# Kernel tuning notes

Measured on AMD Instinct MI355X. Metric: run time of the kernel, lower is better.

Reference implementation:

```python
import jax, jax.numpy as jnp
from jax import lax
import numpy as np

B = 512
IN_CAPS, OUT_CAPS, IN_DIM, OUT_DIM, ITERS = 32 * 6 * 6, 10, 8, 16, 3
EPS = 1e-8


def setup_inputs() -> dict:
    key = jax.random.key(0)
    ks = jax.random.split(key, 12)
    inp = {
        "x": jax.random.normal(ks[0], (B, 1, 28, 28), dtype=jnp.float32),
        "conv1_w": jax.random.normal(ks[1], (256, 1, 9, 9), dtype=jnp.float32) * 0.05,
        "conv1_b": jnp.zeros((256,), dtype=jnp.float32),
        "conv2_w": jax.random.normal(ks[2], (256, 256, 9, 9), dtype=jnp.float32) * 0.02,
        "conv2_b": jnp.zeros((256,), dtype=jnp.float32),
        "W": jax.random.normal(ks[3], (IN_CAPS, OUT_CAPS, IN_DIM, OUT_DIM), dtype=jnp.float32) * 0.1,
        "d1_w": jax.random.normal(ks[4], (OUT_DIM * OUT_CAPS, 512), dtype=jnp.float32) * 0.05,
        "d1_b": jnp.zeros((512,), dtype=jnp.float32),
        "d2_w": jax.random.normal(ks[5], (512, 1024), dtype=jnp.float32) * 0.05,
        "d2_b": jnp.zeros((1024,), dtype=jnp.float32),
        "d3_w": jax.random.normal(ks[6], (1024, 28 * 28), dtype=jnp.float32) * 0.05,
        "d3_b": jnp.zeros((28 * 28,), dtype=jnp.float32),
    }
    return inp


def _squash(s):
    # s2/(1+s2) * s/sqrt(s2+eps), norm over last dim
    s2 = jnp.sum(s * s, axis=-1, keepdims=True)
    return s2 / (1.0 + s2) * (s / jnp.sqrt(s2 + EPS))


def _conv(x, w, b, stride):
    y = lax.conv_general_dilated(x, w, (stride, stride), "VALID",
                                 dimension_numbers=("NCHW", "OIHW", "NCHW"))
    return y + b[None, :, None, None]


def reference(x, conv1_w, conv1_b, conv2_w, conv2_b, W,
              d1_w, d1_b, d2_w, d2_b, d3_w, d3_b):
    h = jax.nn.relu(_conv(x, conv1_w, conv1_b, 1))          # [B,256,20,20]
    h = _conv(h, conv2_w, conv2_b, 2)                       # [B,256,6,6]
    u = h.reshape(h.shape[0], 8, IN_CAPS).transpose(0, 2, 1)  # [B,1152,8]
    u = _squash(u)

    # dynamic routing
    u_hat = jnp.einsum("ijnm,bin->bijm", W, u)              # [B,1152,10,16]
    b_log = jnp.zeros((u.shape[0], IN_CAPS, OUT_CAPS), dtype=u.dtype)
    v = None
    for _ in range(ITERS):
        c = jax.nn.softmax(b_log, axis=1)                   # over in_capsules (as original)
        s = jnp.einsum("bij,bijm->bjm", c, u_hat)           # [B,10,16]
        v = _squash(s)
        b_log = b_log + jnp.einsum("bjm,bijm->bij", v, u_hat)
    caps = v                                                # [B,10,16]

    pred = jnp.argmax(jnp.sum(caps * caps, axis=-1), axis=-1)  # [B]
    mask = jax.lax.stop_gradient(jax.nn.one_hot(pred, OUT_CAPS, dtype=caps.dtype))
    dec_in = (caps * mask[:, :, None]).reshape(caps.shape[0], -1)  # [B,160]
    r = jax.nn.relu(dec_in @ d1_w + d1_b)
    r = jax.nn.relu(r @ d2_w + d2_b)
    r = jax.nn.sigmoid(r @ d3_w + d3_b)
    recon = r.reshape(-1, 1, 28, 28)
    return caps, recon, pred
```

## Files before the change

### kernel.cpp

```cpp
#include <hip/hip_runtime.h>

#define CAPS_EPS 1e-8f

typedef __attribute__((ext_vector_type(8))) short short8;
typedef __attribute__((ext_vector_type(4))) float f32x4;

__device__ inline ushort bf16_rn(float f) {
    uint u = __float_as_uint(f);
    u += 0x7fff + ((u >> 16) & 1);
    return (ushort)(u >> 16);
}
__device__ inline float bf16_f(ushort h) { return __uint_as_float((uint)h << 16); }

__device__ __forceinline__ void gld16(const void* g, void* l) {
    __builtin_amdgcn_global_load_lds(
        (const __attribute__((address_space(1))) unsigned int*)g,
        (__attribute__((address_space(3))) unsigned int*)l, 16, 0, 0);
}


__global__ __launch_bounds__(256) void k_wt2(const float* __restrict__ w2,
                                             ushort* __restrict__ wBhi,
                                             ushort* __restrict__ wBlo) {
    int n = blockIdx.x;
    int c = threadIdx.x;
    const float* src = w2 + (size_t)n * 20736 + c * 81;
    ushort* dh = wBhi + (size_t)n * 20736 + c;
    ushort* dl = wBlo + (size_t)n * 20736 + c;
    for (int t = 0; t < 81; ++t) {
        float f = src[t];
        ushort hi = bf16_rn(f);
        ushort lo = bf16_rn(f - bf16_f(hi));
        dh[t * 256] = hi;
        dl[t * 256] = lo;
    }
}

__global__ __launch_bounds__(256) void k_conv1(const float* __restrict__ x,
                                               const float* __restrict__ w1,
                                               const float* __restrict__ b1,
                                               ushort* __restrict__ h1hi,
                                               ushort* __restrict__ h1lo) {
    int blk = blockIdx.x;
    int b = blk / 5, strip = blk % 5;
    int y0 = strip * 4;
    int c = threadIdx.x;
    float w[81];
#pragma unroll
    for (int k = 0; k < 81; ++k) w[k] = w1[c * 81 + k];
    float bias = b1[c];
    const float* xb = x + (size_t)b * 784;
    for (int dy = 0; dy < 4; ++dy) {
        int y = y0 + dy;
        float acc[20];
#pragma unroll
        for (int i = 0; i < 20; ++i) acc[i] = bias;
#pragma unroll
        for (int ky = 0; ky < 9; ++ky) {
            float xr[28];
            const float4* xp = reinterpret_cast<const float4*>(xb + (y + ky) * 28);
#pragma unroll
            for (int q = 0; q < 7; ++q) {
                float4 v = xp[q];
                xr[q * 4 + 0] = v.x; xr[q * 4 + 1] = v.y;
                xr[q * 4 + 2] = v.z; xr[q * 4 + 3] = v.w;
            }
#pragma unroll
            for (int kx = 0; kx < 9; ++kx) {
                float wv = w[ky * 9 + kx];
#pragma unroll
                for (int xo = 0; xo < 20; ++xo)
                    acc[xo] = fmaf(xr[xo + kx], wv, acc[xo]);
            }
        }
#pragma unroll
        for (int xo = 0; xo < 20; ++xo) {
            float a = fmaxf(acc[xo], 0.f);
            ushort hi = bf16_rn(a);
            ushort lo = bf16_rn(a - bf16_f(hi));
            size_t o = ((size_t)(b * 20 + y) * 20 + xo) * 256 + c;
            h1hi[o] = hi;
            h1lo[o] = lo;
        }
    }
}

__global__ __launch_bounds__(256) void k_h2init(const float* __restrict__ b2,
                                                float* __restrict__ h2) {
    h2[(size_t)blockIdx.x * 256 + threadIdx.x] = b2[threadIdx.x];
}

__global__ __launch_bounds__(256) void k_zero4(float* __restrict__ p) {
    reinterpret_cast<float4*>(p)[(size_t)blockIdx.x * 256 + threadIdx.x] = make_float4(0, 0, 0, 0);
}

__global__ __launch_bounds__(256, 4) void k_conv2m(const ushort* __restrict__ h1hi,
                                                   const ushort* __restrict__ h1lo,
                                                   const ushort* __restrict__ wBhi,
                                                   const ushort* __restrict__ wBlo,
                                                   float* __restrict__ h2) {
    __shared__ ushort Ahi[128 * 32];
    __shared__ ushort Alo[128 * 32];
    __shared__ ushort Bhi[128 * 32];
    __shared__ ushort Blo[128 * 32];
    int tid = threadIdx.x;
    int m0 = blockIdx.x * 128;
    int n0 = blockIdx.y * 128;
    int kbase = blockIdx.z * 2592;

    int wv = tid >> 6, lane = tid & 63;

    int r0 = wv * 32 + (lane >> 2);
    int r1 = r0 + 16;
    int cq = (lane & 3) * 8;
    int mA0 = m0 + r0, mA1 = m0 + r1;
    int mb0 = mA0 / 36, mp0 = mA0 - mb0 * 36;
    int mb1 = mA1 / 36, mp1 = mA1 - mb1 * 36;
    size_t a0 = ((size_t)mb0 * 400 + (mp0 / 6) * 40 + (mp0 % 6) * 2) * 256 + cq;
    size_t a1 = ((size_t)mb1 * 400 + (mp1 / 6) * 40 + (mp1 % 6) * 2) * 256 + cq;
    size_t b0 = (size_t)(n0 + r0) * 20736 + cq;
    size_t b1 = (size_t)(n0 + r1) * 20736 + cq;
    int ldsw = wv * 1024;

    int mhalf = (wv >> 1) * 64, nhalf = (wv & 1) * 64;
    int lrow = lane & 15, quad = lane >> 4;

    f32x4 acc[4][4];
#pragma unroll
    for (int a = 0; a < 4; ++a)
#pragma unroll
        for (int bq = 0; bq < 4; ++bq) acc[a][bq] = (f32x4){0.f, 0.f, 0.f, 0.f};

    for (int ks = 0; ks < 81; ++ks) {
        int k = kbase + ks * 32;
        int t = k >> 8, cc = k & 255;
        int ky = t / 9, kx = t - ky * 9;
        size_t koffA = (size_t)(ky * 5120 + kx * 256 + cc);

        __syncthreads();
        gld16(h1hi + a0 + koffA, &Ahi[ldsw]);
        gld16(h1hi + a1 + koffA, &Ahi[ldsw + 512]);
        gld16(h1lo + a0 + koffA, &Alo[ldsw]);
        gld16(h1lo + a1 + koffA, &Alo[ldsw + 512]);
        gld16(wBhi + b0 + k, &Bhi[ldsw]);
        gld16(wBhi + b1 + k, &Bhi[ldsw + 512]);
        gld16(wBlo + b0 + k, &Blo[ldsw]);
        gld16(wBlo + b1 + k, &Blo[ldsw + 512]);
        __syncthreads();

        short8 bh[4], blo[4];
#pragma unroll
        for (int tn = 0; tn < 4; ++tn) {
            int off = (nhalf + tn * 16 + lrow) * 32 + quad * 8;
            bh[tn] = *reinterpret_cast<short8*>(&Bhi[off]);
            blo[tn] = *reinterpret_cast<short8*>(&Blo[off]);
        }
#pragma unroll
        for (int tm = 0; tm < 4; ++tm) {
            int off = (mhalf + tm * 16 + lrow) * 32 + quad * 8;
            short8 ah = *reinterpret_cast<short8*>(&Ahi[off]);
            short8 al = *reinterpret_cast<short8*>(&Alo[off]);
#pragma unroll
            for (int tn = 0; tn < 4; ++tn) {
                acc[tm][tn] = __builtin_amdgcn_mfma_f32_16x16x32_bf16(ah, bh[tn], acc[tm][tn], 0, 0, 0);
                acc[tm][tn] = __builtin_amdgcn_mfma_f32_16x16x32_bf16(ah, blo[tn], acc[tm][tn], 0, 0, 0);
                acc[tm][tn] = __builtin_amdgcn_mfma_f32_16x16x32_bf16(al, bh[tn], acc[tm][tn], 0, 0, 0);
            }
        }
    }

#pragma unroll
    for (int tm = 0; tm < 4; ++tm) {
        int mrow = m0 + mhalf + tm * 16 + quad * 4;
#pragma unroll
        for (int tn = 0; tn < 4; ++tn) {
            int ncol = n0 + nhalf + tn * 16 + lrow;
#pragma unroll
            for (int r = 0; r < 4; ++r)
                atomicAdd(&h2[(size_t)(mrow + r) * 256 + ncol], acc[tm][tn][r]);
        }
    }
}

__global__ __launch_bounds__(256) void k_squashT(const float* __restrict__ h2,
                                                 float* __restrict__ uT) {
    int i = blockIdx.x;
    int b = blockIdx.y * 256 + threadIdx.x;
    int g = i / 36, s = i - g * 36;
    const float* hp = h2 + ((size_t)b * 36 + s) * 256 + g;
    float val[8];
    float s2 = 0.f;
#pragma unroll
    for (int n = 0; n < 8; ++n) {
        val[n] = hp[n * 32];
        s2 = fmaf(val[n], val[n], s2);
    }
    float scale = s2 / ((1.f + s2) * sqrtf(s2 + CAPS_EPS));
#pragma unroll
    for (int n = 0; n < 8; ++n)
        uT[((size_t)i * 8 + n) * 512 + b] = val[n] * scale;
}

__global__ __launch_bounds__(256) void k_s(const float* __restrict__ Wc,
                                           const float* __restrict__ uT,
                                           const float* __restrict__ bl,
                                           const float* __restrict__ Z,
                                           float* __restrict__ sT,
                                           int first) {
    __shared__ float lw[8 * 1280];
    int tid = threadIdx.x;
    int i0 = blockIdx.x * 8;
    int b = blockIdx.y * 128 + (tid & 127);
    int mh = tid >> 7;
    const float* wg = Wc + (size_t)i0 * 1280;
#pragma unroll
    for (int r = 0; r < 10; ++r) {
        int q4 = (r * 256 + tid) * 4;
        *reinterpret_cast<float4*>(&lw[q4]) = *reinterpret_cast<const float4*>(wg + q4);
    }
    __syncthreads();
    float rzs[10];
    if (!first) {
#pragma unroll
        for (int j = 0; j < 10; ++j) rzs[j] = 1.0f / Z[j * 512 + b];
    }
    float acc[80];
#pragma unroll
    for (int q = 0; q < 80; ++q) acc[q] = 0.f;
    for (int di = 0; di < 8; ++di) {
        int i = i0 + di;
        float ur[8];
#pragma unroll
        for (int n = 0; n < 8; ++n) ur[n] = uT[((size_t)i * 8 + n) * 512 + b];
#pragma unroll
        for (int j = 0; j < 10; ++j) {
            float c;
            if (first) c = (1.0f / 1152.0f);
            else c = expf(bl[((size_t)i * 10 + j) * 512 + b]) * rzs[j];
            const float* wp = &lw[((di * 10 + j) * 8) * 16 + mh * 8];
#pragma unroll
            for (int mm = 0; mm < 8; ++mm) {
                float uh = 0.f;
#pragma unroll
                for (int n = 0; n < 8; ++n) uh = fmaf(wp[n * 16 + mm], ur[n], uh);
                acc[j * 8 + mm] = fmaf(c, uh, acc[j * 8 + mm]);
            }
        }
    }
#pragma unroll
    for (int j = 0; j < 10; ++j)
#pragma unroll
        for (int mm = 0; mm < 8; ++mm)
            atomicAdd(&sT[(j * 16 + mh * 8 + mm) * 512 + b], acc[j * 8 + mm]);
}

__global__ __launch_bounds__(256) void k_v(const float* __restrict__ sT,
                                           float* __restrict__ v,
                                           float* __restrict__ vT,
                                           float* __restrict__ sTz,
                                           float* __restrict__ Z) {
    int idx = blockIdx.x * 256 + threadIdx.x;
    int j = idx >> 9;
    int b = idx & 511;
    float sv[16];
    float s2 = 0.f;
#pragma unroll
    for (int m = 0; m < 16; ++m) {
        sv[m] = sT[(j * 16 + m) * 512 + b];
        s2 = fmaf(sv[m], sv[m], s2);
    }
    float scale = s2 / ((1.f + s2) * sqrtf(s2 + CAPS_EPS));
#pragma unroll
    for (int m = 0; m < 16; ++m) {
        float val = sv[m] * scale;
        v[(size_t)b * 160 + j * 16 + m] = val;
        vT[(j * 16 + m) * 512 + b] = val;
        sTz[(j * 16 + m) * 512 + b] = 0.f;
    }
    Z[idx] = 0.f;
}

__global__ __launch_bounds__(256) void k_bupd(const float* __restrict__ Wc,
                                              const float* __restrict__ uT,
                                              const float* __restrict__ vT,
                                              float* __restrict__ bl,
                                              float* __restrict__ Z) {
    __shared__ float lw[8 * 1280];
    int tid = threadIdx.x;
    int i0 = blockIdx.x * 8;
    int b = blockIdx.y * 128 + (tid & 127);
    int ih = tid >> 7;
    const float* wg = Wc + (size_t)i0 * 1280;
#pragma unroll
    for (int r = 0; r < 10; ++r) {
        int q4 = (r * 256 + tid) * 4;
        *reinterpret_cast<float4*>(&lw[q4]) = *reinterpret_cast<const float4*>(wg + q4);
    }
    __syncthreads();
    float ur[4][8];
#pragma unroll
    for (int ii = 0; ii < 4; ++ii) {
        int i = i0 + ih * 4 + ii;
#pragma unroll
        for (int n = 0; n < 8; ++n) ur[ii][n] = uT[((size_t)i * 8 + n) * 512 + b];
    }
    for (int j = 0; j < 10; ++j) {
        float vj[16];
#pragma unroll
        for (int m = 0; m < 16; ++m) vj[m] = vT[(j * 16 + m) * 512 + b];
        float zp = 0.f;
#pragma unroll
        for (int ii = 0; ii < 4; ++ii) {
            int di = ih * 4 + ii;
            const float* wp = &lw[((di * 10 + j) * 8) * 16];
            float t = 0.f;
#pragma unroll
            for (int n = 0; n < 8; ++n) {
                float wvv = 0.f;
#pragma unroll
                for (int m = 0; m < 16; ++m) wvv = fmaf(wp[n * 16 + m], vj[m], wvv);
                t = fmaf(ur[ii][n], wvv, t);
            }
            size_t idx = ((size_t)(i0 + di) * 10 + j) * 512 + b;
            float nb = bl[idx] + t;
            bl[idx] = nb;
            zp += expf(nb);
        }
        atomicAdd(&Z[j * 512 + b], zp);
    }
}

__global__ __launch_bounds__(256) void k_pred(const float* __restrict__ v,
                                              float* __restrict__ out,
                                              float* __restrict__ dec,
                                              int pred_off) {
    int b = blockIdx.x, t = threadIdx.x;
    __shared__ float sq[160];
    __shared__ float nrm[10];
    __shared__ int ip;
    float val = 0.f;
    if (t < 160) {
        val = v[(size_t)b * 160 + t];
        out[(size_t)b * 160 + t] = val;
        sq[t] = val * val;
    }
    __syncthreads();
    if (t < 10) {
        float s = 0.f;
#pragma unroll
        for (int k = 0; k < 16; ++k) s += sq[t * 16 + k];
        nrm[t] = s;
    }
    __syncthreads();
    if (t == 0) {
        float best = nrm[0];
        int bi = 0;
        for (int j = 1; j < 10; ++j)
            if (nrm[j] > best) { best = nrm[j]; bi = j; }
        ip = bi;
        out[(size_t)pred_off + b] = (float)bi;
    }
    __syncthreads();
    if (t < 160) dec[(size_t)b * 160 + t] = ((t >> 4) == ip) ? val : 0.f;
}

template <int ACT>
__global__ __launch_bounds__(256) void k_gemm(const float* __restrict__ A,
                                              const float* __restrict__ B,
                                              const float* __restrict__ bias,
                                              float* __restrict__ C,
                                              int M, int K, int N) {
    __shared__ float As[16 * 64];
    __shared__ float Bs[16 * 64];
    int tid = threadIdx.x;
    int m0 = blockIdx.y * 64, n0 = blockIdx.x * 64;
    int arow = tid >> 2, akq = (tid & 3) * 4;
    int brow = tid >> 4, bcol = (tid & 15) * 4;
    int ty = tid >> 4, tx = tid & 15;
    float acc[4][4];
#pragma unroll
    for (int r = 0; r < 4; ++r)
#pragma unroll
        for (int q = 0; q < 4; ++q) acc[r][q] = 0.f;
    for (int k0 = 0; k0 < K; k0 += 16) {
        float4 av = *reinterpret_cast<const float4*>(A + (size_t)(m0 + arow) * K + k0 + akq);
        float4 bv = make_float4(0, 0, 0, 0);
        if (n0 + bcol < N)
            bv = *reinterpret_cast<const float4*>(B + (size_t)(k0 + brow) * N + n0 + bcol);
        __syncthreads();
        As[(akq + 0) * 64 + arow] = av.x;
        As[(akq + 1) * 64 + arow] = av.y;
        As[(akq + 2) * 64 + arow] = av.z;
        As[(akq + 3) * 64 + arow] = av.w;
        *reinterpret_cast<float4*>(&Bs[brow * 64 + bcol]) = bv;
        __syncthreads();
#pragma unroll
        for (int kk = 0; kk < 16; ++kk) {
            float4 a4 = *reinterpret_cast<float4*>(&As[kk * 64 + ty * 4]);
            float4 b4 = *reinterpret_cast<float4*>(&Bs[kk * 64 + tx * 4]);
            float ar[4] = {a4.x, a4.y, a4.z, a4.w};
            float br[4] = {b4.x, b4.y, b4.z, b4.w};
#pragma unroll
            for (int r = 0; r < 4; ++r)
#pragma unroll
                for (int q = 0; q < 4; ++q)
                    acc[r][q] = fmaf(ar[r], br[q], acc[r][q]);
        }
    }
#pragma unroll
    for (int r = 0; r < 4; ++r) {
        int mm = m0 + ty * 4 + r;
#pragma unroll
        for (int q = 0; q < 4; ++q) {
            int nn = n0 + tx * 4 + q;
            if (nn < N) {
                float val = acc[r][q] + bias[nn];
                if (ACT == 0) val = fmaxf(val, 0.f);
                else val = 1.f / (1.f + expf(-val));
                C[(size_t)mm * N + nn] = val;
            }
        }
    }
}

extern "C" void kernel_launch(void* const* d_in, const int* in_sizes, int n_in,
                              void* d_out, int out_size, void* d_ws, size_t ws_size,
                              hipStream_t stream) {
    const float* x   = (const float*)d_in[0];
    const float* w1  = (const float*)d_in[1];
    const float* b1  = (const float*)d_in[2];
    const float* w2  = (const float*)d_in[3];
    const float* b2  = (const float*)d_in[4];
    const float* Wc  = (const float*)d_in[5];
    const float* d1w = (const float*)d_in[6];
    const float* d1b = (const float*)d_in[7];
    const float* d2w = (const float*)d_in[8];
    const float* d2b = (const float*)d_in[9];
    const float* d3w = (const float*)d_in[10];
    const float* d3b = (const float*)d_in[11];
    float* out = (float*)d_out;

    ushort* wBhi = (ushort*)d_ws;
    ushort* wBlo = wBhi + 5308416;
    ushort* h1hi = (ushort*)((char*)d_ws + 21233664);
    ushort* h1lo = h1hi + 52428800;
    float*  h2   = (float*)((char*)d_ws + 230948864);

    float* post = (float*)((char*)d_ws + 21233664);
    float* uT  = post + 4718592;
    float* bl  = post + 9437184;
    float* sT  = post + 15335424;
    float* Z   = post + 15417344;
    float* v   = post + 15422464;
    float* vT  = post + 15504384;
    float* dec = post + 15586304;
    float* r1  = post + 15668224;
    float* r2  = post + 15930368;

    int pred_off = out_size - 512;

    k_wt2<<<256, 256, 0, stream>>>(w2, wBhi, wBlo);
    k_conv1<<<2560, 256, 0, stream>>>(x, w1, b1, h1hi, h1lo);
    k_h2init<<<18432, 256, 0, stream>>>(b2, h2);
    k_conv2m<<<dim3(144, 2, 8), 256, 0, stream>>>(h1hi, h1lo, wBhi, wBlo, h2);
    k_zero4<<<5845, 256, 0, stream>>>(bl);
    k_squashT<<<dim3(1152, 2), 256, 0, stream>>>(h2, uT);

    for (int it = 0; it < 3; ++it) {
        k_s<<<dim3(144, 4), 256, 0, stream>>>(Wc, uT, bl, Z, sT, it == 0 ? 1 : 0);
        k_v<<<20, 256, 0, stream>>>(sT, v, vT, sT, Z);
        if (it < 2) k_bupd<<<dim3(144, 4), 256, 0, stream>>>(Wc, uT, vT, bl, Z);
    }

    k_pred<<<512, 256, 0, stream>>>(v, out, dec, pred_off);
    k_gemm<0><<<dim3(8, 8), 256, 0, stream>>>(dec, d1w, d1b, r1, 512, 160, 512);
    k_gemm<0><<<dim3(16, 8), 256, 0, stream>>>(r1, d2w, d2b, r2, 512, 512, 1024);
    k_gemm<1><<<dim3(13, 8), 256, 0, stream>>>(r2, d3w, d3b, out + 81920, 512, 1024, 784);
}
```

Before: 1.649 ms.

## Widen conv2 GEMM tile to cover all 256 output channels per block

The conv2 implicit GEMM block tile grows from 128x128 to 128x256, so each block covers every output channel. Each A (activation) tile is then loaded from global memory once instead of twice, and the grid drops from 2304 to 1152 blocks. The cost is a doubled accumulator array (128 floats per thread), double the B LDS buffers, and launch bounds lowered to 2 blocks per CU. That means higher register pressure and lower occupancy, with only about 4.5 waves of blocks over the CUs.

```diff
diff --git a/kernel.cpp b/kernel.cpp
--- a/kernel.cpp
+++ b/kernel.cpp
@@ -94,42 +94,42 @@
     reinterpret_cast<float4*>(p)[(size_t)blockIdx.x * 256 + threadIdx.x] = make_float4(0, 0, 0, 0);
 }
 
-__global__ __launch_bounds__(256, 4) void k_conv2m(const ushort* __restrict__ h1hi,
+__global__ __launch_bounds__(256, 2) void k_conv2m(const ushort* __restrict__ h1hi,
                                                    const ushort* __restrict__ h1lo,
                                                    const ushort* __restrict__ wBhi,
                                                    const ushort* __restrict__ wBlo,
                                                    float* __restrict__ h2) {
     __shared__ ushort Ahi[128 * 32];
     __shared__ ushort Alo[128 * 32];
-    __shared__ ushort Bhi[128 * 32];
-    __shared__ ushort Blo[128 * 32];
+    __shared__ ushort Bhi[256 * 32];
+    __shared__ ushort Blo[256 * 32];
     int tid = threadIdx.x;
     int m0 = blockIdx.x * 128;
-    int n0 = blockIdx.y * 128;
-    int kbase = blockIdx.z * 2592;
+    int kbase = blockIdx.y * 2592;
 
     int wv = tid >> 6, lane = tid & 63;
-
-    int r0 = wv * 32 + (lane >> 2);
-    int r1 = r0 + 16;
     int cq = (lane & 3) * 8;
-    int mA0 = m0 + r0, mA1 = m0 + r1;
+
+    int ra = wv * 32 + (lane >> 2);
+    int mA0 = m0 + ra, mA1 = mA0 + 16;
     int mb0 = mA0 / 36, mp0 = mA0 - mb0 * 36;
     int mb1 = mA1 / 36, mp1 = mA1 - mb1 * 36;
     size_t a0 = ((size_t)mb0 * 400 + (mp0 / 6) * 40 + (mp0 % 6) * 2) * 256 + cq;
     size_t a1 = ((size_t)mb1 * 400 + (mp1 / 6) * 40 + (mp1 % 6) * 2) * 256 + cq;
-    size_t b0 = (size_t)(n0 + r0) * 20736 + cq;
-    size_t b1 = (size_t)(n0 + r1) * 20736 + cq;
-    int ldsw = wv * 1024;
-
-    int mhalf = (wv >> 1) * 64, nhalf = (wv & 1) * 64;
+    int ldsA = wv * 1024;
+
+    int rb = wv * 64 + (lane >> 2);
+    size_t bB = (size_t)rb * 20736 + cq;
+    int ldsB = wv * 2048;
+
+    int mhalf = (wv >> 1) * 64, nhalf = (wv & 1) * 128;
     int lrow = lane & 15, quad = lane >> 4;
 
-    f32x4 acc[4][4];
+    f32x4 acc[4][8];
 #pragma unroll
     for (int a = 0; a < 4; ++a)
 #pragma unroll
-        for (int bq = 0; bq < 4; ++bq) acc[a][bq] = (f32x4){0.f, 0.f, 0.f, 0.f};
+        for (int bq = 0; bq < 8; ++bq) acc[a][bq] = (f32x4){0.f, 0.f, 0.f, 0.f};
 
     for (int ks = 0; ks < 81; ++ks) {
         int k = kbase + ks * 32;
@@ -138,33 +138,35 @@
         size_t koffA = (size_t)(ky * 5120 + kx * 256 + cc);
 
         __syncthreads();
-        gld16(h1hi + a0 + koffA, &Ahi[ldsw]);
-        gld16(h1hi + a1 + koffA, &Ahi[ldsw + 512]);
-        gld16(h1lo + a0 + koffA, &Alo[ldsw]);
-        gld16(h1lo + a1 + koffA, &Alo[ldsw + 512]);
-        gld16(wBhi + b0 + k, &Bhi[ldsw]);
-        gld16(wBhi + b1 + k, &Bhi[ldsw + 512]);
-        gld16(wBlo + b0 + k, &Blo[ldsw]);
-        gld16(wBlo + b1 + k, &Blo[ldsw + 512]);
+        gld16(h1hi + a0 + koffA, &Ahi[ldsA]);
+        gld16(h1hi + a1 + koffA, &Ahi[ldsA + 512]);
+        gld16(h1lo + a0 + koffA, &Alo[ldsA]);
+        gld16(h1lo + a1 + koffA, &Alo[ldsA + 512]);
+#pragma unroll
+        for (int q = 0; q < 4; ++q) {
+            size_t bo = bB + (size_t)q * 331776 + k;
+            gld16(wBhi + bo, &Bhi[ldsB + q * 512]);
+            gld16(wBlo + bo, &Blo[ldsB + q * 512]);
+        }
         __syncthreads();
 
-        short8 bh[4], blo[4];
-#pragma unroll
-        for (int tn = 0; tn < 4; ++tn) {
-            int off = (nhalf + tn * 16 + lrow) * 32 + quad * 8;
-            bh[tn] = *reinterpret_cast<short8*>(&Bhi[off]);
-            blo[tn] = *reinterpret_cast<short8*>(&Blo[off]);
-        }
+        short8 ah[4], al[4];
 #pragma unroll
         for (int tm = 0; tm < 4; ++tm) {
             int off = (mhalf + tm * 16 + lrow) * 32 + quad * 8;
-            short8 ah = *reinterpret_cast<short8*>(&Ahi[off]);
-            short8 al = *reinterpret_cast<short8*>(&Alo[off]);
-#pragma unroll
-            for (int tn = 0; tn < 4; ++tn) {
-                acc[tm][tn] = __builtin_amdgcn_mfma_f32_16x16x32_bf16(ah, bh[tn], acc[tm][tn], 0, 0, 0);
-                acc[tm][tn] = __builtin_amdgcn_mfma_f32_16x16x32_bf16(ah, blo[tn], acc[tm][tn], 0, 0, 0);
-                acc[tm][tn] = __builtin_amdgcn_mfma_f32_16x16x32_bf16(al, bh[tn], acc[tm][tn], 0, 0, 0);
+            ah[tm] = *reinterpret_cast<short8*>(&Ahi[off]);
+            al[tm] = *reinterpret_cast<short8*>(&Alo[off]);
+        }
+#pragma unroll
+        for (int tn = 0; tn < 8; ++tn) {
+            int off = (nhalf + tn * 16 + lrow) * 32 + quad * 8;
+            short8 bh = *reinterpret_cast<short8*>(&Bhi[off]);
+            short8 bl2 = *reinterpret_cast<short8*>(&Blo[off]);
+#pragma unroll
+            for (int tm = 0; tm < 4; ++tm) {
+                acc[tm][tn] = __builtin_amdgcn_mfma_f32_16x16x32_bf16(ah[tm], bh, acc[tm][tn], 0, 0, 0);
+                acc[tm][tn] = __builtin_amdgcn_mfma_f32_16x16x32_bf16(ah[tm], bl2, acc[tm][tn], 0, 0, 0);
+                acc[tm][tn] = __builtin_amdgcn_mfma_f32_16x16x32_bf16(al[tm], bh, acc[tm][tn], 0, 0, 0);
             }
         }
     }
@@ -173,8 +175,8 @@
     for (int tm = 0; tm < 4; ++tm) {
         int mrow = m0 + mhalf + tm * 16 + quad * 4;
 #pragma unroll
-        for (int tn = 0; tn < 4; ++tn) {
-            int ncol = n0 + nhalf + tn * 16 + lrow;
+        for (int tn = 0; tn < 8; ++tn) {
+            int ncol = nhalf + tn * 16 + lrow;
 #pragma unroll
             for (int r = 0; r < 4; ++r)
                 atomicAdd(&h2[(size_t)(mrow + r) * 256 + ncol], acc[tm][tn][r]);
@@ -462,7 +464,7 @@
     k_wt2<<<256, 256, 0, stream>>>(w2, wBhi, wBlo);
     k_conv1<<<2560, 256, 0, stream>>>(x, w1, b1, h1hi, h1lo);
     k_h2init<<<18432, 256, 0, stream>>>(b2, h2);
-    k_conv2m<<<dim3(144, 2, 8), 256, 0, stream>>>(h1hi, h1lo, wBhi, wBlo, h2);
+    k_conv2m<<<dim3(144, 8), 256, 0, stream>>>(h1hi, h1lo, wBhi, wBlo, h2);
     k_zero4<<<5845, 256, 0, stream>>>(bl);
     k_squashT<<<dim3(1152, 2), 256, 0, stream>>>(h2, uT);
 
```

After: 1.419 ms. 1.16x faster.
